# Kernel optimization log

Measured on AMD Instinct MI355X. Metric: run time of the kernel, lower is better.

Reference implementation:

```python
import jax, jax.numpy as jnp
import numpy as np

DEPTH = 17                      # tree depth (root at level 0)
D_IN = 128                      # input embedding dim
H = 128                         # hidden dim
N = 2 ** (DEPTH + 1) - 1        # total nodes in complete binary tree, level-major order


def setup_inputs() -> dict:
    key = jax.random.key(0)
    ks = jax.random.split(key, 13)
    s = 0.05
    inp = {"x": jax.random.normal(ks[0], (N, D_IN), jnp.float32)}
    # nn.Linear params; W stored as (in, out) so y = x @ W + b
    gate_names = ["i", "f", "o", "u"]
    for g, k in zip(gate_names, range(1, 5)):
        k1, k2, k3 = jax.random.split(ks[k], 3)
        inp[f"W_{g}"] = jax.random.normal(k1, (D_IN, H), jnp.float32) * s
        inp[f"b_{g}"] = jax.random.normal(k2, (H,), jnp.float32) * s
        inp[f"U_{g}"] = jax.random.normal(k3, (H, H), jnp.float32) * s
    inp["depth"] = DEPTH
    return inp


def reference(x, W_i, b_i, U_i, W_f, b_f, U_f, W_o, b_o, U_o, W_u, b_u, U_u, depth):
    # Precompute input contributions for ALL nodes in one GEMM per gate.
    Xi = x @ W_i + b_i  # [N, H]
    Xf = x @ W_f + b_f
    Xo = x @ W_o + b_o
    Xu = x @ W_u + b_u

    def lvl(l):
        return 2 ** l - 1, 2 ** l  # (start offset, n nodes) at level l

    # Leaves (level = depth): no children -> h_tilde = 0, c = i*u
    s0, n0 = lvl(depth)
    i = jax.nn.sigmoid(Xi[s0:s0 + n0])
    o = jax.nn.sigmoid(Xo[s0:s0 + n0])
    u = jnp.tanh(Xu[s0:s0 + n0])
    c = i * u
    h = o * jnp.tanh(c)

    # Process levels bottom-up; every internal node has exactly 2 children
    for l in range(depth - 1, -1, -1):
        sl, nl = lvl(l)
        ch = h.reshape(nl, 2, H)   # child hidden states per parent
        cc = c.reshape(nl, 2, H)   # child cell states per parent
        h_tilde = ch.sum(axis=1)   # child-sum
        i = jax.nn.sigmoid(Xi[sl:sl + nl] + h_tilde @ U_i)
        o = jax.nn.sigmoid(Xo[sl:sl + nl] + h_tilde @ U_o)
        u = jnp.tanh(Xu[sl:sl + nl] + h_tilde @ U_u)
        # per-child forget gates: f_j = sigmoid(W_f x + U_f h_j)
        f = jax.nn.sigmoid(Xf[sl:sl + nl][:, None, :] + ch @ U_f)  # [nl, 2, H]
        c = i * u + (f * cc).sum(axis=1)
        h = o * jnp.tanh(c)

    # Root (hidden, cell) stacked as [2, H]
    return jnp.stack([h[0], c[0]])
```

## Files before the change

### kernel.cpp

```cpp
#include <hip/hip_runtime.h>
#include <hip/hip_bf16.h>


typedef __bf16 bf16_t;
typedef __bf16 bf16x8 __attribute__((ext_vector_type(8)));
typedef float  f32x4  __attribute__((ext_vector_type(4)));

#define MFMA16(a, b, c) __builtin_amdgcn_mfma_f32_16x16x32_bf16((a), (b), (c), 0, 0, 0)

__device__ __forceinline__ float rcp_(float x) { return __builtin_amdgcn_rcpf(x); }
__device__ __forceinline__ float sigm(float x) { return rcp_(1.0f + __expf(-x)); }
__device__ __forceinline__ float tanh_(float x) {
    float a = fabsf(x);
    float e = __expf(2.0f * a);
    float t = fmaf(-2.0f, rcp_(e + 1.0f), 1.0f);
    return copysignf(t, x);
}

__device__ __forceinline__ void cvt16(const float* __restrict__ src, bf16_t* __restrict__ dst)
{
    float tmp[16];
    *(float4*)&tmp[0]  = ((const float4*)src)[0];
    *(float4*)&tmp[4]  = ((const float4*)src)[1];
    *(float4*)&tmp[8]  = ((const float4*)src)[2];
    *(float4*)&tmp[12] = ((const float4*)src)[3];
    bf16_t b[16];
#pragma unroll
    for (int j = 0; j < 16; j++) b[j] = (bf16_t)tmp[j];
    *(bf16x8*)&dst[0] = *(bf16x8*)&b[0];
    *(bf16x8*)&dst[8] = *(bf16x8*)&b[8];
}

__device__ __forceinline__ void zero16(bf16_t* __restrict__ dst)
{
    bf16x8 z = (bf16x8)(bf16_t)0.f;
    *(bf16x8*)&dst[0] = z;
    *(bf16x8*)&dst[8] = z;
}

__global__ __launch_bounds__(256)
void k_prep(const float* __restrict__ Wi, const float* __restrict__ Wf,
            const float* __restrict__ Wo, const float* __restrict__ Wu,
            const float* __restrict__ Ui, const float* __restrict__ Uf,
            const float* __restrict__ Uo, const float* __restrict__ Uu,
            bf16_t* __restrict__ SW)
{
    int b = blockIdx.x;
    const float* src;
    switch (b) {
        case 0: src = Wi; break; case 1: src = Wf; break;
        case 2: src = Wo; break; case 3: src = Wu; break;
        case 4: src = Ui; break; case 5: src = Uf; break;
        case 6: src = Uo; break; default: src = Uu; break;
    }
    if (b < 4) {
        bf16_t* hi = SW + (size_t)b * 16384;
        for (int idx = threadIdx.x; idx < 16384; idx += 256) {
            int j = idx & 7, ln = (idx >> 3) & 63, kb = (idx >> 9) & 3, nt = idx >> 11;
            int k = kb * 32 + (ln >> 4) * 8 + j;
            int n = nt * 16 + (ln & 15);
            hi[idx] = (bf16_t)src[k * 128 + n];
        }
    } else {
        bf16_t* hi = SW + 65536 + (size_t)(b - 4) * 32768;
        bf16_t* lo = hi + 16384;
        for (int idx = threadIdx.x; idx < 16384; idx += 256) {
            int j = idx & 7, ln = (idx >> 3) & 63, kb = (idx >> 9) & 3, nt = idx >> 11;
            int k = kb * 32 + (ln >> 4) * 8 + j;
            int n = nt * 16 + (ln & 15);
            float w = src[k * 128 + n];
            bf16_t hh = (bf16_t)w;
            hi[idx] = hh;
            lo[idx] = (bf16_t)(w - (float)hh);
        }
    }
}

__device__ __forceinline__ void leaf32(
    const float* __restrict__ x, const bf16_t* __restrict__ SW,
    const float* __restrict__ bi, const float* __restrict__ bo,
    const float* __restrict__ bu,
    bf16_t (* __restrict__ XA)[136],
    bf16_t (* __restrict__ BH)[136], bf16_t (* __restrict__ BC)[136],
    int xRowBase, int valid, int outRowOff, int tid)
{
    {
        int r = tid >> 3, cb = (tid & 7) * 16;
        if (r < valid) cvt16(x + (size_t)(xRowBase + r - 1) * 128 + cb, &XA[r][cb]);
        else           zero16(&XA[r][cb]);
    }
    __syncthreads();
    const int wave = tid >> 6, lane = tid & 63;
    const int quad = lane >> 4, lc = lane & 15;

    f32x4 aI[2][2], aO[2][2], aU[2][2];
#pragma unroll
    for (int nt = 0; nt < 2; nt++)
#pragma unroll
        for (int mt = 0; mt < 2; mt++) {
            aI[nt][mt] = (f32x4){0.f, 0.f, 0.f, 0.f};
            aO[nt][mt] = (f32x4){0.f, 0.f, 0.f, 0.f};
            aU[nt][mt] = (f32x4){0.f, 0.f, 0.f, 0.f};
        }
    for (int kb = 0; kb < 4; kb++) {
        const int k0 = kb * 32 + quad * 8;
        bf16x8 a0 = *(const bf16x8*)&XA[lc][k0];
        bf16x8 a1 = *(const bf16x8*)&XA[16 + lc][k0];
#pragma unroll
        for (int nt = 0; nt < 2; nt++) {
            const size_t boff = ((size_t)((2 * wave + nt) * 4 + kb) * 64 + lane) * 8;
            bf16x8 bWi = *(const bf16x8*)(SW + boff);
            bf16x8 bWo = *(const bf16x8*)(SW + 32768 + boff);
            bf16x8 bWu = *(const bf16x8*)(SW + 49152 + boff);
            aI[nt][0] = MFMA16(a0, bWi, aI[nt][0]);
            aI[nt][1] = MFMA16(a1, bWi, aI[nt][1]);
            aO[nt][0] = MFMA16(a0, bWo, aO[nt][0]);
            aO[nt][1] = MFMA16(a1, bWo, aO[nt][1]);
            aU[nt][0] = MFMA16(a0, bWu, aU[nt][0]);
            aU[nt][1] = MFMA16(a1, bWu, aU[nt][1]);
        }
    }
#pragma unroll
    for (int nt = 0; nt < 2; nt++) {
        const int col = (2 * wave + nt) * 16 + lc;
        float bii = bi[col], boi = bo[col], bui = bu[col];
#pragma unroll
        for (int mt = 0; mt < 2; mt++)
#pragma unroll
            for (int r = 0; r < 4; r++) {
                float iv = sigm(aI[nt][mt][r] + bii);
                float ov = sigm(aO[nt][mt][r] + boi);
                float uv = tanh_(aU[nt][mt][r] + bui);
                float cv = iv * uv;
                int pl = mt * 16 + quad * 4 + r;
                BH[outRowOff + pl][col] = (bf16_t)(ov * tanh_(cv));
                BC[outRowOff + pl][col] = (bf16_t)cv;
            }
    }
    __syncthreads();
}

__device__ __forceinline__ void compute32(
    const float* __restrict__ x, const bf16_t* __restrict__ SW,
    const float* __restrict__ bi, const float* __restrict__ bf_,
    const float* __restrict__ bo, const float* __restrict__ bu,
    bf16_t (* __restrict__ XA)[136], float (* __restrict__ SC)[132],
    const bf16_t (* __restrict__ CH)[136],
    const float* __restrict__ Cglob, int ccBase,
    const bf16_t (* __restrict__ BCc)[136], bool ccLds,
    int xRowBase, int valid,
    bf16_t (* __restrict__ BHo)[136], bf16_t (* __restrict__ BCo)[136], int outRowOff,
    bf16_t* __restrict__ Hg, float* __restrict__ Cg, int outBase,
    bf16_t (* __restrict__ Hd)[136], bool outLds, int tid)
{
    {
        int r = tid >> 3, cb = (tid & 7) * 16;
        if (r < valid) cvt16(x + (size_t)(xRowBase + r - 1) * 128 + cb, &XA[r][cb]);
        else           zero16(&XA[r][cb]);
    }
    __syncthreads();

    const int wave = tid >> 6, lane = tid & 63;
    const int quad = lane >> 4, lc = lane & 15;

    f32x4 aI[2][2], aO[2][2], aU[2][2], aXf[2][2], aF[2][4];
#pragma unroll
    for (int nt = 0; nt < 2; nt++) {
#pragma unroll
        for (int mt = 0; mt < 2; mt++) {
            aI[nt][mt]  = (f32x4){0.f, 0.f, 0.f, 0.f};
            aO[nt][mt]  = (f32x4){0.f, 0.f, 0.f, 0.f};
            aU[nt][mt]  = (f32x4){0.f, 0.f, 0.f, 0.f};
            aXf[nt][mt] = (f32x4){0.f, 0.f, 0.f, 0.f};
        }
#pragma unroll
        for (int mt = 0; mt < 4; mt++) aF[nt][mt] = (f32x4){0.f, 0.f, 0.f, 0.f};
    }

    for (int kb = 0; kb < 4; kb++) {
        const int k0 = kb * 32 + quad * 8;
        bf16x8 xa0 = *(const bf16x8*)&XA[lc][k0];
        bf16x8 xa1 = *(const bf16x8*)&XA[16 + lc][k0];
        bf16x8 h00 = *(const bf16x8*)&CH[2 * lc][k0];
        bf16x8 h01 = *(const bf16x8*)&CH[2 * lc + 1][k0];
        bf16x8 h10 = *(const bf16x8*)&CH[2 * lc + 32][k0];
        bf16x8 h11 = *(const bf16x8*)&CH[2 * lc + 33][k0];
        bf16x8 at0, at1;
#pragma unroll
        for (int j = 0; j < 8; j++) {
            at0[j] = (bf16_t)((float)h00[j] + (float)h01[j]);
            at1[j] = (bf16_t)((float)h10[j] + (float)h11[j]);
        }
        bf16x8 ac0 = *(const bf16x8*)&CH[lc][k0];
        bf16x8 ac1 = *(const bf16x8*)&CH[16 + lc][k0];
        bf16x8 ac2 = *(const bf16x8*)&CH[32 + lc][k0];
        bf16x8 ac3 = *(const bf16x8*)&CH[48 + lc][k0];
#pragma unroll
        for (int nt = 0; nt < 2; nt++) {
            const size_t boff = ((size_t)((2 * wave + nt) * 4 + kb) * 64 + lane) * 8;
            bf16x8 bWi = *(const bf16x8*)(SW + boff);
            bf16x8 bWf = *(const bf16x8*)(SW + 16384 + boff);
            bf16x8 bWo = *(const bf16x8*)(SW + 32768 + boff);
            bf16x8 bWu = *(const bf16x8*)(SW + 49152 + boff);
            aI[nt][0]  = MFMA16(xa0, bWi, aI[nt][0]);
            aI[nt][1]  = MFMA16(xa1, bWi, aI[nt][1]);
            aXf[nt][0] = MFMA16(xa0, bWf, aXf[nt][0]);
            aXf[nt][1] = MFMA16(xa1, bWf, aXf[nt][1]);
            aO[nt][0]  = MFMA16(xa0, bWo, aO[nt][0]);
            aO[nt][1]  = MFMA16(xa1, bWo, aO[nt][1]);
            aU[nt][0]  = MFMA16(xa0, bWu, aU[nt][0]);
            aU[nt][1]  = MFMA16(xa1, bWu, aU[nt][1]);
            const bf16_t* Ub = SW + 65536;
            bf16x8 bIh = *(const bf16x8*)(Ub + boff);
            bf16x8 bIl = *(const bf16x8*)(Ub + 16384 + boff);
            aI[nt][0] = MFMA16(at0, bIh, aI[nt][0]);
            aI[nt][0] = MFMA16(at0, bIl, aI[nt][0]);
            aI[nt][1] = MFMA16(at1, bIh, aI[nt][1]);
            aI[nt][1] = MFMA16(at1, bIl, aI[nt][1]);
            bf16x8 bOh = *(const bf16x8*)(Ub + 65536 + boff);
            bf16x8 bOl = *(const bf16x8*)(Ub + 81920 + boff);
            aO[nt][0] = MFMA16(at0, bOh, aO[nt][0]);
            aO[nt][0] = MFMA16(at0, bOl, aO[nt][0]);
            aO[nt][1] = MFMA16(at1, bOh, aO[nt][1]);
            aO[nt][1] = MFMA16(at1, bOl, aO[nt][1]);
            bf16x8 bUh = *(const bf16x8*)(Ub + 98304 + boff);
            bf16x8 bUl = *(const bf16x8*)(Ub + 114688 + boff);
            aU[nt][0] = MFMA16(at0, bUh, aU[nt][0]);
            aU[nt][0] = MFMA16(at0, bUl, aU[nt][0]);
            aU[nt][1] = MFMA16(at1, bUh, aU[nt][1]);
            aU[nt][1] = MFMA16(at1, bUl, aU[nt][1]);
            bf16x8 bFh = *(const bf16x8*)(Ub + 32768 + boff);
            bf16x8 bFl = *(const bf16x8*)(Ub + 49152 + boff);
            aF[nt][0] = MFMA16(ac0, bFh, aF[nt][0]);
            aF[nt][0] = MFMA16(ac0, bFl, aF[nt][0]);
            aF[nt][1] = MFMA16(ac1, bFh, aF[nt][1]);
            aF[nt][1] = MFMA16(ac1, bFl, aF[nt][1]);
            aF[nt][2] = MFMA16(ac2, bFh, aF[nt][2]);
            aF[nt][2] = MFMA16(ac2, bFl, aF[nt][2]);
            aF[nt][3] = MFMA16(ac3, bFh, aF[nt][3]);
            aF[nt][3] = MFMA16(ac3, bFl, aF[nt][3]);
        }
    }
    __syncthreads();

#pragma unroll
    for (int nt = 0; nt < 2; nt++) {
        const int col = (2 * wave + nt) * 16 + lc;
        float bfv = bf_[col];
#pragma unroll
        for (int mt = 0; mt < 2; mt++)
#pragma unroll
            for (int r = 0; r < 4; r++)
                SC[mt * 16 + quad * 4 + r][col] = aXf[nt][mt][r] + bfv;
    }
    __syncthreads();

    float Sv[2][4][2];
#pragma unroll
    for (int nt = 0; nt < 2; nt++) {
        const int col = (2 * wave + nt) * 16 + lc;
#pragma unroll
        for (int mt = 0; mt < 4; mt++)
#pragma unroll
            for (int pi = 0; pi < 2; pi++) {
                int pl = mt * 8 + quad * 2 + pi;
                float xf = SC[pl][col];
                float f0 = sigm(xf + aF[nt][mt][2 * pi]);
                float f1 = sigm(xf + aF[nt][mt][2 * pi + 1]);
                float c0, c1;
                if (ccLds) {
                    c0 = (float)BCc[2 * pl][col];
                    c1 = (float)BCc[2 * pl + 1][col];
                } else {
                    size_t cr = (size_t)(ccBase + 2 * pl) * 128 + col;
                    c0 = Cglob[cr];
                    c1 = Cglob[cr + 128];
                }
                Sv[nt][mt][pi] = f0 * c0 + f1 * c1;
            }
    }
    __syncthreads();
#pragma unroll
    for (int nt = 0; nt < 2; nt++) {
        const int col = (2 * wave + nt) * 16 + lc;
#pragma unroll
        for (int mt = 0; mt < 4; mt++)
#pragma unroll
            for (int pi = 0; pi < 2; pi++)
                SC[mt * 8 + quad * 2 + pi][col] = Sv[nt][mt][pi];
    }
    __syncthreads();

    float hr[2][2][4];
#pragma unroll
    for (int nt = 0; nt < 2; nt++) {
        const int col = (2 * wave + nt) * 16 + lc;
        float bii = bi[col], boi = bo[col], bui = bu[col];
#pragma unroll
        for (int mt = 0; mt < 2; mt++)
#pragma unroll
            for (int r = 0; r < 4; r++) {
                int pl = mt * 16 + quad * 4 + r;
                float iv = sigm(aI[nt][mt][r] + bii);
                float ov = sigm(aO[nt][mt][r] + boi);
                float uv = tanh_(aU[nt][mt][r] + bui);
                float cv = iv * uv + SC[pl][col];
                float hv = ov * tanh_(cv);
                hr[nt][mt][r] = hv;
                if (outLds) {
                    BHo[outRowOff + pl][col] = (bf16_t)hv;
                    BCo[outRowOff + pl][col] = (bf16_t)cv;
                } else if (pl < valid) {
                    Cg[(size_t)(outBase + pl) * 128 + col] = cv;
                }
            }
    }
    if (outLds) {
        __syncthreads();
    } else {
        __syncthreads();
#pragma unroll
        for (int nt = 0; nt < 2; nt++) {
            const int col = (2 * wave + nt) * 16 + lc;
#pragma unroll
            for (int mt = 0; mt < 2; mt++)
#pragma unroll
                for (int r = 0; r < 4; r++)
                    Hd[mt * 16 + quad * 4 + r][col] = (bf16_t)hr[nt][mt][r];
        }
        __syncthreads();
        int r = tid >> 3, cb = (tid & 7) * 16;
        if (r < valid) {
            uint4* dst = (uint4*)(Hg + (size_t)(outBase + r) * 128 + cb);
            dst[0] = *(uint4*)&Hd[r][cb];
            dst[1] = *(uint4*)&Hd[r][cb + 8];
        }
        __syncthreads();
    }
}

__global__ __launch_bounds__(256)
void k_pair(const float* __restrict__ x, const bf16_t* __restrict__ SW,
            const float* __restrict__ bi, const float* __restrict__ bf_,
            const float* __restrict__ bo, const float* __restrict__ bu,
            bf16_t* __restrict__ H, float* __restrict__ C,
            int Pa, int leafB)
{
    __shared__ __align__(16) char smem[60928];
    bf16_t (*XA)[136] = (bf16_t(*)[136])(smem);
    bf16_t (*HC)[136] = (bf16_t(*)[136])(smem + 8704);
    float  (*SC)[132] = (float(*)[132])(smem);
    bf16_t (*BH)[136] = (bf16_t(*)[136])(smem + 26112);
    bf16_t (*BC)[136] = (bf16_t(*)[136])(smem + 43520);

    const int tid = threadIdx.x;
    const int t   = blockIdx.x;
    const int sA0 = Pa + 32 * t;
    int Pta = Pa - 32 * t; if (Pta > 32) Pta = 32;

    if (Pta < 32) {
        bf16x8 z = (bf16x8)(bf16_t)0.f;
        for (int i = tid; i < 64 * 17; i += 256) {
            ((bf16x8*)BH)[i] = z;
            ((bf16x8*)BC)[i] = z;
        }
    }

    for (int q = 0; q < 2; q++) {
        int bvalid = 2 * Pa - (64 * t + 32 * q);
        if (bvalid > 32) bvalid = 32;
        if (bvalid <= 0) break;
        if (leafB) {
            leaf32(x, SW, bi, bo, bu, XA, BH, BC,
                   2 * sA0 + 32 * q, bvalid, 32 * q, tid);
        } else {
            {
                int r = tid >> 2, cb = (tid & 3) * 32;
                if (r < 2 * bvalid) {
                    const uint4* src = (const uint4*)(H + (size_t)(4 * sA0 + 64 * q + r) * 128 + cb);
                    *(uint4*)&HC[r][cb]      = src[0];
                    *(uint4*)&HC[r][cb + 8]  = src[1];
                    *(uint4*)&HC[r][cb + 16] = src[2];
                    *(uint4*)&HC[r][cb + 24] = src[3];
                } else {
                    uint4 z = {0u, 0u, 0u, 0u};
                    *(uint4*)&HC[r][cb]      = z;
                    *(uint4*)&HC[r][cb + 8]  = z;
                    *(uint4*)&HC[r][cb + 16] = z;
                    *(uint4*)&HC[r][cb + 24] = z;
                }
            }
            compute32(x, SW, bi, bf_, bo, bu, XA, SC,
                      (const bf16_t(*)[136])HC,
                      C, 4 * sA0 + 64 * q, nullptr, false,
                      2 * sA0 + 32 * q, bvalid,
                      BH, BC, 32 * q,
                      nullptr, nullptr, 0, nullptr, true, tid);
        }
    }

    compute32(x, SW, bi, bf_, bo, bu, XA, SC,
              (const bf16_t(*)[136])BH,
              nullptr, 0, (const bf16_t(*)[136])BC, true,
              sA0, Pta,
              nullptr, nullptr, 0,
              H, C, sA0, HC, false, tid);
}

__global__ __launch_bounds__(256, 2)
void k_lvl(const float* __restrict__ x, const bf16_t* __restrict__ SW,
           const float* __restrict__ bi, const float* __restrict__ bf_,
           const float* __restrict__ bo, const float* __restrict__ bu,
           bf16_t* H, float* C, int np)
{
    __shared__ __align__(16) char smem[75264];
    f32x4  (*PR)[4][64] = (f32x4(*)[4][64])smem;
    bf16_t (*XA)[136]   = (bf16_t(*)[136])(smem + 49152);
    bf16_t (*CH)[136]   = (bf16_t(*)[136])(smem + 57856);
    float  (*SC)[17]    = (float(*)[17])smem;

    const int tid = threadIdx.x;
    const int wave = tid >> 6, lane = tid & 63;
    const int quad = lane >> 4, lc = lane & 15;

    const int task = blockIdx.x;
    const int ct = task & 7, mt = task >> 3;
    int valid = np - 32 * mt; if (valid > 32) valid = 32;
    if (valid <= 0) return;
    const int prow = np + 32 * mt;
    const int crow = 2 * np + 64 * mt;

    {
        int r = tid >> 3, cb = (tid & 7) * 16;
        if (r < valid) cvt16(x + (size_t)(prow - 1 + r) * 128 + cb, &XA[r][cb]);
        else           zero16(&XA[r][cb]);
    }
    {
        int r = tid >> 2, cb = (tid & 3) * 32;
        if (r < 2 * valid) {
            const uint4* src = (const uint4*)(H + (size_t)(crow + r) * 128 + cb);
            *(uint4*)&CH[r][cb]      = src[0];
            *(uint4*)&CH[r][cb + 8]  = src[1];
            *(uint4*)&CH[r][cb + 16] = src[2];
            *(uint4*)&CH[r][cb + 24] = src[3];
        } else {
            uint4 z = {0u, 0u, 0u, 0u};
            *(uint4*)&CH[r][cb]      = z;
            *(uint4*)&CH[r][cb + 8]  = z;
            *(uint4*)&CH[r][cb + 16] = z;
            *(uint4*)&CH[r][cb + 24] = z;
        }
    }
    __syncthreads();

    f32x4 z4 = (f32x4){0.f, 0.f, 0.f, 0.f};
    f32x4 aI0 = z4, aI1 = z4, aXf0 = z4, aXf1 = z4;
    f32x4 aO0 = z4, aO1 = z4, aU0 = z4, aU1 = z4;
    f32x4 aF0 = z4, aF1 = z4, aF2 = z4, aF3 = z4;
    {
        const int k0 = wave * 32 + quad * 8;
        bf16x8 xa0 = *(const bf16x8*)&XA[lc][k0];
        bf16x8 xa1 = *(const bf16x8*)&XA[16 + lc][k0];
        bf16x8 h00 = *(const bf16x8*)&CH[2 * lc][k0];
        bf16x8 h01 = *(const bf16x8*)&CH[2 * lc + 1][k0];
        bf16x8 h10 = *(const bf16x8*)&CH[2 * lc + 32][k0];
        bf16x8 h11 = *(const bf16x8*)&CH[2 * lc + 33][k0];
        bf16x8 at0, at1;
#pragma unroll
        for (int j = 0; j < 8; j++) {
            at0[j] = (bf16_t)((float)h00[j] + (float)h01[j]);
            at1[j] = (bf16_t)((float)h10[j] + (float)h11[j]);
        }
        bf16x8 ac0 = *(const bf16x8*)&CH[lc][k0];
        bf16x8 ac1 = *(const bf16x8*)&CH[16 + lc][k0];
        bf16x8 ac2 = *(const bf16x8*)&CH[32 + lc][k0];
        bf16x8 ac3 = *(const bf16x8*)&CH[48 + lc][k0];

        const size_t boff = ((size_t)(ct * 4 + wave) * 64 + lane) * 8;
        bf16x8 bWi = *(const bf16x8*)(SW + boff);
        bf16x8 bWf = *(const bf16x8*)(SW + 16384 + boff);
        bf16x8 bWo = *(const bf16x8*)(SW + 32768 + boff);
        bf16x8 bWu = *(const bf16x8*)(SW + 49152 + boff);
        const bf16_t* Ub = SW + 65536;
        bf16x8 bIh = *(const bf16x8*)(Ub + boff);
        bf16x8 bIl = *(const bf16x8*)(Ub + 16384 + boff);
        bf16x8 bFh = *(const bf16x8*)(Ub + 32768 + boff);
        bf16x8 bFl = *(const bf16x8*)(Ub + 49152 + boff);
        bf16x8 bOh = *(const bf16x8*)(Ub + 65536 + boff);
        bf16x8 bOl = *(const bf16x8*)(Ub + 81920 + boff);
        bf16x8 bUh = *(const bf16x8*)(Ub + 98304 + boff);
        bf16x8 bUl = *(const bf16x8*)(Ub + 114688 + boff);

        aI0  = MFMA16(xa0, bWi, aI0);  aI1  = MFMA16(xa1, bWi, aI1);
        aXf0 = MFMA16(xa0, bWf, aXf0); aXf1 = MFMA16(xa1, bWf, aXf1);
        aO0  = MFMA16(xa0, bWo, aO0);  aO1  = MFMA16(xa1, bWo, aO1);
        aU0  = MFMA16(xa0, bWu, aU0);  aU1  = MFMA16(xa1, bWu, aU1);
        aI0 = MFMA16(at0, bIh, aI0); aI0 = MFMA16(at0, bIl, aI0);
        aI1 = MFMA16(at1, bIh, aI1); aI1 = MFMA16(at1, bIl, aI1);
        aO0 = MFMA16(at0, bOh, aO0); aO0 = MFMA16(at0, bOl, aO0);
        aO1 = MFMA16(at1, bOh, aO1); aO1 = MFMA16(at1, bOl, aO1);
        aU0 = MFMA16(at0, bUh, aU0); aU0 = MFMA16(at0, bUl, aU0);
        aU1 = MFMA16(at1, bUh, aU1); aU1 = MFMA16(at1, bUl, aU1);
        aF0 = MFMA16(ac0, bFh, aF0); aF0 = MFMA16(ac0, bFl, aF0);
        aF1 = MFMA16(ac1, bFh, aF1); aF1 = MFMA16(ac1, bFl, aF1);
        aF2 = MFMA16(ac2, bFh, aF2); aF2 = MFMA16(ac2, bFl, aF2);
        aF3 = MFMA16(ac3, bFh, aF3); aF3 = MFMA16(ac3, bFl, aF3);
    }
    if (wave != 0) {
        PR[0][wave][lane]  = aI0;  PR[1][wave][lane]  = aI1;
        PR[2][wave][lane]  = aXf0; PR[3][wave][lane]  = aXf1;
        PR[4][wave][lane]  = aO0;  PR[5][wave][lane]  = aO1;
        PR[6][wave][lane]  = aU0;  PR[7][wave][lane]  = aU1;
        PR[8][wave][lane]  = aF0;  PR[9][wave][lane]  = aF1;
        PR[10][wave][lane] = aF2;  PR[11][wave][lane] = aF3;
    }
    __syncthreads();
    if (wave == 0) {
        aI0  += PR[0][1][lane]  + PR[0][2][lane]  + PR[0][3][lane];
        aI1  += PR[1][1][lane]  + PR[1][2][lane]  + PR[1][3][lane];
        aXf0 += PR[2][1][lane]  + PR[2][2][lane]  + PR[2][3][lane];
        aXf1 += PR[3][1][lane]  + PR[3][2][lane]  + PR[3][3][lane];
        aO0  += PR[4][1][lane]  + PR[4][2][lane]  + PR[4][3][lane];
        aO1  += PR[5][1][lane]  + PR[5][2][lane]  + PR[5][3][lane];
        aU0  += PR[6][1][lane]  + PR[6][2][lane]  + PR[6][3][lane];
        aU1  += PR[7][1][lane]  + PR[7][2][lane]  + PR[7][3][lane];
        aF0  += PR[8][1][lane]  + PR[8][2][lane]  + PR[8][3][lane];
        aF1  += PR[9][1][lane]  + PR[9][2][lane]  + PR[9][3][lane];
        aF2  += PR[10][1][lane] + PR[10][2][lane] + PR[10][3][lane];
        aF3  += PR[11][1][lane] + PR[11][2][lane] + PR[11][3][lane];

        const int colg = ct * 16 + lc;
        float c0v[4][2], c1v[4][2];
#pragma unroll
        for (int m2 = 0; m2 < 4; m2++)
#pragma unroll
            for (int pi = 0; pi < 2; pi++) {
                int pl = m2 * 8 + quad * 2 + pi;
                size_t cr = (size_t)(crow + 2 * pl) * 128 + colg;
                c0v[m2][pi] = C[cr];
                c1v[m2][pi] = C[cr + 128];
            }
        float bfv = bf_[colg];
#pragma unroll
        for (int r = 0; r < 4; r++) {
            SC[quad * 4 + r][lc]      = aXf0[r] + bfv;
            SC[16 + quad * 4 + r][lc] = aXf1[r] + bfv;
        }
#define NS_FPATH(M2, AF)                                            \
        _Pragma("unroll")                                           \
        for (int pi = 0; pi < 2; pi++) {                            \
            int pl = M2 * 8 + quad * 2 + pi;                        \
            float xf = SC[pl][lc];                                  \
            float f0 = sigm(xf + AF[2 * pi]);                       \
            float f1 = sigm(xf + AF[2 * pi + 1]);                   \
            SC[pl][lc] = f0 * c0v[M2][pi] + f1 * c1v[M2][pi];       \
        }
        NS_FPATH(0, aF0) NS_FPATH(1, aF1) NS_FPATH(2, aF2) NS_FPATH(3, aF3)
#undef NS_FPATH
        float bii = bi[colg], boi = bo[colg], bui = bu[colg];
#define NS_IOU(MT, AI, AO, AU)                                      \
        _Pragma("unroll")                                           \
        for (int r = 0; r < 4; r++) {                               \
            int pl = MT * 16 + quad * 4 + r;                        \
            float iv = sigm(AI[r] + bii);                           \
            float ov = sigm(AO[r] + boi);                           \
            float uv = tanh_(AU[r] + bui);                          \
            float cv = iv * uv + SC[pl][lc];                        \
            if (pl < valid) {                                       \
                H[(size_t)(prow + pl) * 128 + colg] = (bf16_t)(ov * tanh_(cv)); \
                C[(size_t)(prow + pl) * 128 + colg] = cv;           \
            }                                                       \
        }
        NS_IOU(0, aI0, aO0, aU0)
        NS_IOU(1, aI1, aO1, aU1)
#undef NS_IOU
    }
}

__global__ __launch_bounds__(256)
void k_out(const bf16_t* __restrict__ H, const float* __restrict__ C,
           float* __restrict__ out)
{
    int t = threadIdx.x;
    if (t < 128)      out[t] = (float)H[128 + t];
    else if (t < 256) out[t] = C[t];
}

extern "C" void kernel_launch(void* const* d_in, const int* in_sizes, int n_in,
                              void* d_out, int out_size, void* d_ws, size_t ws_size,
                              hipStream_t stream)
{
    const float* x   = (const float*)d_in[0];
    const float* Wi  = (const float*)d_in[1];
    const float* bi  = (const float*)d_in[2];
    const float* Ui  = (const float*)d_in[3];
    const float* Wf  = (const float*)d_in[4];
    const float* bf_ = (const float*)d_in[5];
    const float* Uf  = (const float*)d_in[6];
    const float* Wo  = (const float*)d_in[7];
    const float* bo  = (const float*)d_in[8];
    const float* Uo  = (const float*)d_in[9];
    const float* Wu  = (const float*)d_in[10];
    const float* bu  = (const float*)d_in[11];
    const float* Uu  = (const float*)d_in[12];

    int Ntot  = in_sizes[0] / 128;
    int depth = 31 - __builtin_clz((unsigned)(Ntot + 1)) - 1;

    char* w = (char*)d_ws;
    bf16_t* SW = (bf16_t*)w;  w += 393216;
    bf16_t* H  = (bf16_t*)w;  w += (size_t)(Ntot + 1) * 128 * sizeof(bf16_t);
    float*  C  = (float*)w;

    k_prep<<<8, 256, 0, stream>>>(Wi, Wf, Wo, Wu, Ui, Uf, Uo, Uu, SW);

    {
        int Pa = 1 << (depth - 1);
        int blocks = (Pa + 31) / 32;
        k_pair<<<blocks, 256, 0, stream>>>(x, SW, bi, bf_, bo, bu, H, C, Pa, 1);
    }
    int lowest = depth - 1;
    for (int A = depth - 3; A >= 14; A -= 2) {
        int Pa = 1 << A;
        int blocks = (Pa + 31) / 32;
        k_pair<<<blocks, 256, 0, stream>>>(x, SW, bi, bf_, bo, bu, H, C, Pa, 0);
        lowest = A;
    }
    for (int l = lowest - 1; l >= 0; l--) {
        int np = 1 << l;
        int nmt = (np + 31) / 32;
        k_lvl<<<nmt * 8, 256, 0, stream>>>(x, SW, bi, bf_, bo, bu, H, C, np);
    }
    k_out<<<1, 256, 0, stream>>>(H, C, (float*)d_out);
}
```

Baseline: 511.7 us.

## Replace fused two-level pair kernels with standalone leaf kernel plus per-level launches

Removes the k_pair kernel, which fused two tree levels per launch and kept the intermediate level in shared memory, and adds a dedicated k_leaf kernel that computes all leaves and writes H (bf16) and C (fp32) to global memory. Every internal level is then handled by the generic per-level k_lvl kernel. This simplifies the schedule and lets the leaf kernel run at higher occupancy (launch bounds 4 blocks per CU, smaller shared memory) without edge guards. The cost is extra global round trips of H and C for the lower levels and more kernel launches.

```diff
diff --git a/kernel.cpp b/kernel.cpp
--- a/kernel.cpp
+++ b/kernel.cpp
@@ -76,18 +76,22 @@
     }
 }
 
-__device__ __forceinline__ void leaf32(
-    const float* __restrict__ x, const bf16_t* __restrict__ SW,
-    const float* __restrict__ bi, const float* __restrict__ bo,
-    const float* __restrict__ bu,
-    bf16_t (* __restrict__ XA)[136],
-    bf16_t (* __restrict__ BH)[136], bf16_t (* __restrict__ BC)[136],
-    int xRowBase, int valid, int outRowOff, int tid)
-{
+__global__ __launch_bounds__(256, 4)
+void k_leaf(const float* __restrict__ x, const bf16_t* __restrict__ SW,
+            const float* __restrict__ bi, const float* __restrict__ bo,
+            const float* __restrict__ bu,
+            bf16_t* __restrict__ H, float* __restrict__ C, int np)
+{
+    __shared__ __align__(16) char smem[34816];
+    bf16_t (*XA)[136] = (bf16_t(*)[136])smem;
+    bf16_t (*Hd)[136] = (bf16_t(*)[136])(smem + 8704);
+    float  (*Cd)[136] = (float(*)[136])(smem + 17408);
+
+    const int tid = threadIdx.x;
+    const int srow = np + 32 * blockIdx.x;
     {
         int r = tid >> 3, cb = (tid & 7) * 16;
-        if (r < valid) cvt16(x + (size_t)(xRowBase + r - 1) * 128 + cb, &XA[r][cb]);
-        else           zero16(&XA[r][cb]);
+        cvt16(x + (size_t)(srow - 1 + r) * 128 + cb, &XA[r][cb]);
     }
     __syncthreads();
     const int wave = tid >> 6, lane = tid & 63;
@@ -102,6 +106,7 @@
             aO[nt][mt] = (f32x4){0.f, 0.f, 0.f, 0.f};
             aU[nt][mt] = (f32x4){0.f, 0.f, 0.f, 0.f};
         }
+#pragma unroll
     for (int kb = 0; kb < 4; kb++) {
         const int k0 = kb * 32 + quad * 8;
         bf16x8 a0 = *(const bf16x8*)&XA[lc][k0];
@@ -120,6 +125,7 @@
             aU[nt][1] = MFMA16(a1, bWu, aU[nt][1]);
         }
     }
+    __syncthreads();
 #pragma unroll
     for (int nt = 0; nt < 2; nt++) {
         const int col = (2 * wave + nt) * 16 + lc;
@@ -133,278 +139,20 @@
                 float uv = tanh_(aU[nt][mt][r] + bui);
                 float cv = iv * uv;
                 int pl = mt * 16 + quad * 4 + r;
-                BH[outRowOff + pl][col] = (bf16_t)(ov * tanh_(cv));
-                BC[outRowOff + pl][col] = (bf16_t)cv;
+                Hd[pl][col] = (bf16_t)(ov * tanh_(cv));
+                Cd[pl][col] = cv;
             }
     }
     __syncthreads();
-}
-
-__device__ __forceinline__ void compute32(
-    const float* __restrict__ x, const bf16_t* __restrict__ SW,
-    const float* __restrict__ bi, const float* __restrict__ bf_,
-    const float* __restrict__ bo, const float* __restrict__ bu,
-    bf16_t (* __restrict__ XA)[136], float (* __restrict__ SC)[132],
-    const bf16_t (* __restrict__ CH)[136],
-    const float* __restrict__ Cglob, int ccBase,
-    const bf16_t (* __restrict__ BCc)[136], bool ccLds,
-    int xRowBase, int valid,
-    bf16_t (* __restrict__ BHo)[136], bf16_t (* __restrict__ BCo)[136], int outRowOff,
-    bf16_t* __restrict__ Hg, float* __restrict__ Cg, int outBase,
-    bf16_t (* __restrict__ Hd)[136], bool outLds, int tid)
-{
     {
         int r = tid >> 3, cb = (tid & 7) * 16;
-        if (r < valid) cvt16(x + (size_t)(xRowBase + r - 1) * 128 + cb, &XA[r][cb]);
-        else           zero16(&XA[r][cb]);
-    }
-    __syncthreads();
-
-    const int wave = tid >> 6, lane = tid & 63;
-    const int quad = lane >> 4, lc = lane & 15;
-
-    f32x4 aI[2][2], aO[2][2], aU[2][2], aXf[2][2], aF[2][4];
-#pragma unroll
-    for (int nt = 0; nt < 2; nt++) {
-#pragma unroll
-        for (int mt = 0; mt < 2; mt++) {
-            aI[nt][mt]  = (f32x4){0.f, 0.f, 0.f, 0.f};
-            aO[nt][mt]  = (f32x4){0.f, 0.f, 0.f, 0.f};
-            aU[nt][mt]  = (f32x4){0.f, 0.f, 0.f, 0.f};
-            aXf[nt][mt] = (f32x4){0.f, 0.f, 0.f, 0.f};
-        }
-#pragma unroll
-        for (int mt = 0; mt < 4; mt++) aF[nt][mt] = (f32x4){0.f, 0.f, 0.f, 0.f};
-    }
-
-    for (int kb = 0; kb < 4; kb++) {
-        const int k0 = kb * 32 + quad * 8;
-        bf16x8 xa0 = *(const bf16x8*)&XA[lc][k0];
-        bf16x8 xa1 = *(const bf16x8*)&XA[16 + lc][k0];
-        bf16x8 h00 = *(const bf16x8*)&CH[2 * lc][k0];
-        bf16x8 h01 = *(const bf16x8*)&CH[2 * lc + 1][k0];
-        bf16x8 h10 = *(const bf16x8*)&CH[2 * lc + 32][k0];
-        bf16x8 h11 = *(const bf16x8*)&CH[2 * lc + 33][k0];
-        bf16x8 at0, at1;
-#pragma unroll
-        for (int j = 0; j < 8; j++) {
-            at0[j] = (bf16_t)((float)h00[j] + (float)h01[j]);
-            at1[j] = (bf16_t)((float)h10[j] + (float)h11[j]);
-        }
-        bf16x8 ac0 = *(const bf16x8*)&CH[lc][k0];
-        bf16x8 ac1 = *(const bf16x8*)&CH[16 + lc][k0];
-        bf16x8 ac2 = *(const bf16x8*)&CH[32 + lc][k0];
-        bf16x8 ac3 = *(const bf16x8*)&CH[48 + lc][k0];
-#pragma unroll
-        for (int nt = 0; nt < 2; nt++) {
-            const size_t boff = ((size_t)((2 * wave + nt) * 4 + kb) * 64 + lane) * 8;
-            bf16x8 bWi = *(const bf16x8*)(SW + boff);
-            bf16x8 bWf = *(const bf16x8*)(SW + 16384 + boff);
-            bf16x8 bWo = *(const bf16x8*)(SW + 32768 + boff);
-            bf16x8 bWu = *(const bf16x8*)(SW + 49152 + boff);
-            aI[nt][0]  = MFMA16(xa0, bWi, aI[nt][0]);
-            aI[nt][1]  = MFMA16(xa1, bWi, aI[nt][1]);
-            aXf[nt][0] = MFMA16(xa0, bWf, aXf[nt][0]);
-            aXf[nt][1] = MFMA16(xa1, bWf, aXf[nt][1]);
-            aO[nt][0]  = MFMA16(xa0, bWo, aO[nt][0]);
-            aO[nt][1]  = MFMA16(xa1, bWo, aO[nt][1]);
-            aU[nt][0]  = MFMA16(xa0, bWu, aU[nt][0]);
-            aU[nt][1]  = MFMA16(xa1, bWu, aU[nt][1]);
-            const bf16_t* Ub = SW + 65536;
-            bf16x8 bIh = *(const bf16x8*)(Ub + boff);
-            bf16x8 bIl = *(const bf16x8*)(Ub + 16384 + boff);
-            aI[nt][0] = MFMA16(at0, bIh, aI[nt][0]);
-            aI[nt][0] = MFMA16(at0, bIl, aI[nt][0]);
-            aI[nt][1] = MFMA16(at1, bIh, aI[nt][1]);
-            aI[nt][1] = MFMA16(at1, bIl, aI[nt][1]);
-            bf16x8 bOh = *(const bf16x8*)(Ub + 65536 + boff);
-            bf16x8 bOl = *(const bf16x8*)(Ub + 81920 + boff);
-            aO[nt][0] = MFMA16(at0, bOh, aO[nt][0]);
-            aO[nt][0] = MFMA16(at0, bOl, aO[nt][0]);
-            aO[nt][1] = MFMA16(at1, bOh, aO[nt][1]);
-            aO[nt][1] = MFMA16(at1, bOl, aO[nt][1]);
-            bf16x8 bUh = *(const bf16x8*)(Ub + 98304 + boff);
-            bf16x8 bUl = *(const bf16x8*)(Ub + 114688 + boff);
-            aU[nt][0] = MFMA16(at0, bUh, aU[nt][0]);
-            aU[nt][0] = MFMA16(at0, bUl, aU[nt][0]);
-            aU[nt][1] = MFMA16(at1, bUh, aU[nt][1]);
-            aU[nt][1] = MFMA16(at1, bUl, aU[nt][1]);
-            bf16x8 bFh = *(const bf16x8*)(Ub + 32768 + boff);
-            bf16x8 bFl = *(const bf16x8*)(Ub + 49152 + boff);
-            aF[nt][0] = MFMA16(ac0, bFh, aF[nt][0]);
-            aF[nt][0] = MFMA16(ac0, bFl, aF[nt][0]);
-            aF[nt][1] = MFMA16(ac1, bFh, aF[nt][1]);
-            aF[nt][1] = MFMA16(ac1, bFl, aF[nt][1]);
-            aF[nt][2] = MFMA16(ac2, bFh, aF[nt][2]);
-            aF[nt][2] = MFMA16(ac2, bFl, aF[nt][2]);
-            aF[nt][3] = MFMA16(ac3, bFh, aF[nt][3]);
-            aF[nt][3] = MFMA16(ac3, bFl, aF[nt][3]);
-        }
-    }
-    __syncthreads();
-
-#pragma unroll
-    for (int nt = 0; nt < 2; nt++) {
-        const int col = (2 * wave + nt) * 16 + lc;
-        float bfv = bf_[col];
-#pragma unroll
-        for (int mt = 0; mt < 2; mt++)
-#pragma unroll
-            for (int r = 0; r < 4; r++)
-                SC[mt * 16 + quad * 4 + r][col] = aXf[nt][mt][r] + bfv;
-    }
-    __syncthreads();
-
-    float Sv[2][4][2];
-#pragma unroll
-    for (int nt = 0; nt < 2; nt++) {
-        const int col = (2 * wave + nt) * 16 + lc;
-#pragma unroll
-        for (int mt = 0; mt < 4; mt++)
-#pragma unroll
-            for (int pi = 0; pi < 2; pi++) {
-                int pl = mt * 8 + quad * 2 + pi;
-                float xf = SC[pl][col];
-                float f0 = sigm(xf + aF[nt][mt][2 * pi]);
-                float f1 = sigm(xf + aF[nt][mt][2 * pi + 1]);
-                float c0, c1;
-                if (ccLds) {
-                    c0 = (float)BCc[2 * pl][col];
-                    c1 = (float)BCc[2 * pl + 1][col];
-                } else {
-                    size_t cr = (size_t)(ccBase + 2 * pl) * 128 + col;
-                    c0 = Cglob[cr];
-                    c1 = Cglob[cr + 128];
-                }
-                Sv[nt][mt][pi] = f0 * c0 + f1 * c1;
-            }
-    }
-    __syncthreads();
-#pragma unroll
-    for (int nt = 0; nt < 2; nt++) {
-        const int col = (2 * wave + nt) * 16 + lc;
-#pragma unroll
-        for (int mt = 0; mt < 4; mt++)
-#pragma unroll
-            for (int pi = 0; pi < 2; pi++)
-                SC[mt * 8 + quad * 2 + pi][col] = Sv[nt][mt][pi];
-    }
-    __syncthreads();
-
-    float hr[2][2][4];
-#pragma unroll
-    for (int nt = 0; nt < 2; nt++) {
-        const int col = (2 * wave + nt) * 16 + lc;
-        float bii = bi[col], boi = bo[col], bui = bu[col];
-#pragma unroll
-        for (int mt = 0; mt < 2; mt++)
-#pragma unroll
-            for (int r = 0; r < 4; r++) {
-                int pl = mt * 16 + quad * 4 + r;
-                float iv = sigm(aI[nt][mt][r] + bii);
-                float ov = sigm(aO[nt][mt][r] + boi);
-                float uv = tanh_(aU[nt][mt][r] + bui);
-                float cv = iv * uv + SC[pl][col];
-                float hv = ov * tanh_(cv);
-                hr[nt][mt][r] = hv;
-                if (outLds) {
-                    BHo[outRowOff + pl][col] = (bf16_t)hv;
-                    BCo[outRowOff + pl][col] = (bf16_t)cv;
-                } else if (pl < valid) {
-                    Cg[(size_t)(outBase + pl) * 128 + col] = cv;
-                }
-            }
-    }
-    if (outLds) {
-        __syncthreads();
-    } else {
-        __syncthreads();
-#pragma unroll
-        for (int nt = 0; nt < 2; nt++) {
-            const int col = (2 * wave + nt) * 16 + lc;
-#pragma unroll
-            for (int mt = 0; mt < 2; mt++)
-#pragma unroll
-                for (int r = 0; r < 4; r++)
-                    Hd[mt * 16 + quad * 4 + r][col] = (bf16_t)hr[nt][mt][r];
-        }
-        __syncthreads();
-        int r = tid >> 3, cb = (tid & 7) * 16;
-        if (r < valid) {
-            uint4* dst = (uint4*)(Hg + (size_t)(outBase + r) * 128 + cb);
-            dst[0] = *(uint4*)&Hd[r][cb];
-            dst[1] = *(uint4*)&Hd[r][cb + 8];
-        }
-        __syncthreads();
-    }
-}
-
-__global__ __launch_bounds__(256)
-void k_pair(const float* __restrict__ x, const bf16_t* __restrict__ SW,
-            const float* __restrict__ bi, const float* __restrict__ bf_,
-            const float* __restrict__ bo, const float* __restrict__ bu,
-            bf16_t* __restrict__ H, float* __restrict__ C,
-            int Pa, int leafB)
-{
-    __shared__ __align__(16) char smem[60928];
-    bf16_t (*XA)[136] = (bf16_t(*)[136])(smem);
-    bf16_t (*HC)[136] = (bf16_t(*)[136])(smem + 8704);
-    float  (*SC)[132] = (float(*)[132])(smem);
-    bf16_t (*BH)[136] = (bf16_t(*)[136])(smem + 26112);
-    bf16_t (*BC)[136] = (bf16_t(*)[136])(smem + 43520);
-
-    const int tid = threadIdx.x;
-    const int t   = blockIdx.x;
-    const int sA0 = Pa + 32 * t;
-    int Pta = Pa - 32 * t; if (Pta > 32) Pta = 32;
-
-    if (Pta < 32) {
-        bf16x8 z = (bf16x8)(bf16_t)0.f;
-        for (int i = tid; i < 64 * 17; i += 256) {
-            ((bf16x8*)BH)[i] = z;
-            ((bf16x8*)BC)[i] = z;
-        }
-    }
-
-    for (int q = 0; q < 2; q++) {
-        int bvalid = 2 * Pa - (64 * t + 32 * q);
-        if (bvalid > 32) bvalid = 32;
-        if (bvalid <= 0) break;
-        if (leafB) {
-            leaf32(x, SW, bi, bo, bu, XA, BH, BC,
-                   2 * sA0 + 32 * q, bvalid, 32 * q, tid);
-        } else {
-            {
-                int r = tid >> 2, cb = (tid & 3) * 32;
-                if (r < 2 * bvalid) {
-                    const uint4* src = (const uint4*)(H + (size_t)(4 * sA0 + 64 * q + r) * 128 + cb);
-                    *(uint4*)&HC[r][cb]      = src[0];
-                    *(uint4*)&HC[r][cb + 8]  = src[1];
-                    *(uint4*)&HC[r][cb + 16] = src[2];
-                    *(uint4*)&HC[r][cb + 24] = src[3];
-                } else {
-                    uint4 z = {0u, 0u, 0u, 0u};
-                    *(uint4*)&HC[r][cb]      = z;
-                    *(uint4*)&HC[r][cb + 8]  = z;
-                    *(uint4*)&HC[r][cb + 16] = z;
-                    *(uint4*)&HC[r][cb + 24] = z;
-                }
-            }
-            compute32(x, SW, bi, bf_, bo, bu, XA, SC,
-                      (const bf16_t(*)[136])HC,
-                      C, 4 * sA0 + 64 * q, nullptr, false,
-                      2 * sA0 + 32 * q, bvalid,
-                      BH, BC, 32 * q,
-                      nullptr, nullptr, 0, nullptr, true, tid);
-        }
-    }
-
-    compute32(x, SW, bi, bf_, bo, bu, XA, SC,
-              (const bf16_t(*)[136])BH,
-              nullptr, 0, (const bf16_t(*)[136])BC, true,
-              sA0, Pta,
-              nullptr, nullptr, 0,
-              H, C, sA0, HC, false, tid);
+        uint4* dh = (uint4*)(H + (size_t)(srow + r) * 128 + cb);
+        dh[0] = *(uint4*)&Hd[r][cb];
+        dh[1] = *(uint4*)&Hd[r][cb + 8];
+        float4* dc = (float4*)(C + (size_t)(srow + r) * 128 + cb);
+        const float4* sc4 = (const float4*)&Cd[r][cb];
+        dc[0] = sc4[0]; dc[1] = sc4[1]; dc[2] = sc4[2]; dc[3] = sc4[3];
+    }
 }
 
 __global__ __launch_bounds__(256, 2)
@@ -614,19 +362,10 @@
 
     k_prep<<<8, 256, 0, stream>>>(Wi, Wf, Wo, Wu, Ui, Uf, Uo, Uu, SW);
 
-    {
-        int Pa = 1 << (depth - 1);
-        int blocks = (Pa + 31) / 32;
-        k_pair<<<blocks, 256, 0, stream>>>(x, SW, bi, bf_, bo, bu, H, C, Pa, 1);
-    }
-    int lowest = depth - 1;
-    for (int A = depth - 3; A >= 14; A -= 2) {
-        int Pa = 1 << A;
-        int blocks = (Pa + 31) / 32;
-        k_pair<<<blocks, 256, 0, stream>>>(x, SW, bi, bf_, bo, bu, H, C, Pa, 0);
-        lowest = A;
-    }
-    for (int l = lowest - 1; l >= 0; l--) {
+    int NL = 1 << depth;
+    k_leaf<<<NL / 32, 256, 0, stream>>>(x, SW, bi, bo, bu, H, C, NL);
+
+    for (int l = depth - 1; l >= 0; l--) {
         int np = 1 << l;
         int nmt = (np + 31) / 32;
         k_lvl<<<nmt * 8, 256, 0, stream>>>(x, SW, bi, bf_, bo, bu, H, C, np);
```

After: 701.0 us. 1.37x slower.
